# Kernel optimization log

Hardware: AMD Instinct MI355X
Metric: run time of the kernel (lower is better)

The kernel has to match this reference:

```python
import jax, jax.numpy as jnp
import numpy as np

B, S, D = 8, 1024, 768
H, DH = 8, 96          # number_of_heads, head_outdim = D // H
DFF = 4 * D            # mlp hidden
EPS = 1e-5


def _p(key, shape, scale=0.02):
    return (jax.random.normal(key, shape, dtype=jnp.float32) * scale)


def setup_inputs() -> dict:
    key = jax.random.key(0)
    ks = jax.random.split(key, 16)
    return {
        "h": jax.random.normal(ks[0], (B, S, D), dtype=jnp.float32),
        "x": jax.random.normal(ks[1], (B, S, D), dtype=jnp.float32),
        # SLN 1: scalar gamma/beta + LayerNorm affine
        "g1": jnp.ones((), jnp.float32), "be1": jnp.zeros((), jnp.float32),
        "ln1_w": jnp.ones((D,), jnp.float32), "ln1_b": jnp.zeros((D,), jnp.float32),
        # SLN 2
        "g2": jnp.ones((), jnp.float32), "be2": jnp.zeros((), jnp.float32),
        "ln2_w": jnp.ones((D,), jnp.float32), "ln2_b": jnp.zeros((D,), jnp.float32),
        # MSA projections (stored as [in, out] for x @ W)
        "Wq": _p(ks[2], (D, H * DH)), "bq": jnp.zeros((H * DH,), jnp.float32),
        "Wk": _p(ks[3], (D, H * DH)), "bk": jnp.zeros((H * DH,), jnp.float32),
        "Wv": _p(ks[4], (D, H * DH)), "bv": jnp.zeros((H * DH,), jnp.float32),
        "Wo": _p(ks[5], (H * DH, D)), "bo": jnp.zeros((D,), jnp.float32),
        # MLP: D -> 4D -> D, relu
        "W1": _p(ks[6], (D, DFF)), "b1": jnp.zeros((DFF,), jnp.float32),
        "W2": _p(ks[7], (DFF, D)), "b2": jnp.zeros((D,), jnp.float32),
    }


def _sln(h, x, gamma, beta, w, b):
    # SLN(h, x) = gamma * x * LayerNorm(h) + beta * x
    mu = jnp.mean(h, axis=-1, keepdims=True)
    var = jnp.var(h, axis=-1, keepdims=True)
    ln = (h - mu) * jax.lax.rsqrt(var + EPS) * w + b
    return gamma * x * ln + beta * x


def _l2_msa(h, Wq, bq, Wk, bk, Wv, bv, Wo, bo):
    # L2-distance multi-head self-attention (lp=2)
    def heads(W, bias):
        y = h @ W + bias                      # [B,S,H*DH]
        return y.reshape(B, S, H, DH).transpose(0, 2, 1, 3)  # [B,H,S,DH]
    q, k, v = heads(Wq, bq), heads(Wk, bk), heads(Wv, bv)
    # pairwise L2 distances via the quadratic expansion (avoids [B,H,S,S,DH])
    q2 = jnp.sum(q * q, axis=-1)              # [B,H,S]
    k2 = jnp.sum(k * k, axis=-1)              # [B,H,S]
    qk = jnp.einsum("bhsd,bhtd->bhst", q, k)  # [B,H,S,S]
    d2 = jnp.maximum(q2[..., :, None] + k2[..., None, :] - 2.0 * qk, 0.0)
    dist = jnp.sqrt(d2)                       # cdist(q, k, p=2)
    attn = jax.nn.softmax(-dist / np.sqrt(DH), axis=-1)
    out = jnp.einsum("bhst,bhtd->bhsd", attn, v)  # [B,H,S,DH]
    out = out.transpose(0, 2, 1, 3).reshape(B, S, H * DH)
    return out @ Wo + bo


def reference(h, x, g1, be1, ln1_w, ln1_b, g2, be2, ln2_w, ln2_b,
              Wq, bq, Wk, bk, Wv, bv, Wo, bo, W1, b1, W2, b2):
    h1 = _sln(h, x, g1, be1, ln1_w, ln1_b)
    htmp = _l2_msa(h1, Wq, bq, Wk, bk, Wv, bv, Wo, bo) + h   # dropout_rate=0 -> identity
    h2 = _sln(htmp, x, g2, be2, ln2_w, ln2_b)
    hf = jax.nn.relu(h2 @ W1 + b1) @ W2 + b2 + htmp
    return (x, hf)
```

## Files before the change

kernel.cpp:

```cpp
#include <hip/hip_runtime.h>
#include <math.h>

#define B_ 8
#define S_ 1024
#define D_ 768
#define H_ 8
#define DH_ 96
#define DFF_ 3072
#define NTOK (B_*S_)
#define QKVW 2304
#define EPS_ 1e-5f

typedef __attribute__((ext_vector_type(4))) float f4;
typedef __attribute__((ext_vector_type(4))) int i4;
typedef __attribute__((ext_vector_type(8))) __bf16 bf16x8;
typedef __attribute__((ext_vector_type(4))) unsigned short us4;
typedef __attribute__((ext_vector_type(8))) unsigned short us8;

static __device__ __forceinline__ unsigned short f2bf(float f) {
    unsigned int u = __builtin_bit_cast(unsigned int, f);
    u += 0x7fffu + ((u >> 16) & 1u);
    return (unsigned short)(u >> 16);
}
static __device__ __forceinline__ float bf2f(unsigned short u) {
    unsigned int x = ((unsigned int)u) << 16;
    return __builtin_bit_cast(float, x);
}

#define GLOBAL_LOAD_LDS16(g, l) \
    __builtin_amdgcn_global_load_lds((const __attribute__((address_space(1))) unsigned int*)(g), \
                                     (__attribute__((address_space(3))) unsigned int*)(l), 16, 0, 0)

__global__ __launch_bounds__(192) void sln_kernel(
    const float* __restrict__ h, const float* __restrict__ x,
    const float* __restrict__ gamma, const float* __restrict__ beta,
    const float* __restrict__ w, const float* __restrict__ bvec,
    unsigned short* __restrict__ out_bf, float* __restrict__ xcopy)
{
    int row = blockIdx.x;
    int t = threadIdx.x;
    const float4* h4 = (const float4*)(h + (size_t)row * D_);
    const float4* x4 = (const float4*)(x + (size_t)row * D_);
    float4 hv = h4[t];
    float s  = hv.x + hv.y + hv.z + hv.w;
    float ss = hv.x*hv.x + hv.y*hv.y + hv.z*hv.z + hv.w*hv.w;
    #pragma unroll
    for (int off = 32; off > 0; off >>= 1) {
        s  += __shfl_down(s, off);
        ss += __shfl_down(ss, off);
    }
    __shared__ float red[2][3];
    int wid = t >> 6;
    if ((t & 63) == 0) { red[0][wid] = s; red[1][wid] = ss; }
    __syncthreads();
    float sum   = red[0][0] + red[0][1] + red[0][2];
    float sumsq = red[1][0] + red[1][1] + red[1][2];
    float mu  = sum * (1.0f / D_);
    float var = sumsq * (1.0f / D_) - mu * mu;
    float rstd = rsqrtf(var + EPS_);
    float g = gamma[0], be = beta[0];
    float4 wv = ((const float4*)w)[t];
    float4 bv = ((const float4*)bvec)[t];
    float4 xv = x4[t];
    us4 o;
    o.x = f2bf(xv.x * (g * ((hv.x - mu) * rstd * wv.x + bv.x) + be));
    o.y = f2bf(xv.y * (g * ((hv.y - mu) * rstd * wv.y + bv.y) + be));
    o.z = f2bf(xv.z * (g * ((hv.z - mu) * rstd * wv.z + bv.z) + be));
    o.w = f2bf(xv.w * (g * ((hv.w - mu) * rstd * wv.w + bv.w) + be));
    *(us4*)(out_bf + (size_t)row * D_ + t * 4) = o;
    if (xcopy) ((float4*)(xcopy + (size_t)row * D_))[t] = xv;
}

__global__ __launch_bounds__(256) void prep_all_kernel(
    const float* __restrict__ Wq, const float* __restrict__ Wk,
    const float* __restrict__ Wv, const float* __restrict__ Wo,
    const float* __restrict__ W1, const float* __restrict__ W2,
    const float* __restrict__ bq, const float* __restrict__ bk, const float* __restrict__ bv,
    unsigned short* __restrict__ Wqkvt, unsigned short* __restrict__ Wot,
    unsigned short* __restrict__ W1t, unsigned short* __restrict__ W2t,
    float* __restrict__ bqkv)
{
    int id = blockIdx.x;
    int tx = threadIdx.x, ty = threadIdx.y;
    if (id >= 6912) {
        int i = (id - 6912) * 256 + ty * 32 + tx;
        if (i < QKVW) {
            float v = (i < 768) ? bq[i] : (i < 1536) ? bk[i - 768] : bv[i - 1536];
            bqkv[i] = v;
        }
        return;
    }
    const float* in; unsigned short* out; int K, N, nbx, rel;
    if (id < 1728)      { int m = id / 576; rel = id % 576;
                          in = (m == 0) ? Wq : (m == 1) ? Wk : Wv;
                          out = Wqkvt + (size_t)m * 768 * 768; K = 768; N = 768; nbx = 24; }
    else if (id < 2304) { rel = id - 1728; in = Wo; out = Wot;  K = 768;  N = 768;  nbx = 24; }
    else if (id < 4608) { rel = id - 2304; in = W1; out = W1t;  K = 768;  N = 3072; nbx = 96; }
    else                { rel = id - 4608; in = W2; out = W2t;  K = 3072; N = 768;  nbx = 24; }
    int n0 = (rel % nbx) * 32, k0 = (rel / nbx) * 32;
    __shared__ float tile[32][33];
    #pragma unroll
    for (int r = 0; r < 4; r++)
        tile[ty + r * 8][tx] = in[(size_t)(k0 + ty + r * 8) * N + n0 + tx];
    __syncthreads();
    #pragma unroll
    for (int r = 0; r < 4; r++)
        out[(size_t)(n0 + ty + r * 8) * K + k0 + tx] = f2bf(tile[tx][ty + r * 8]);
}

template<int OUT_BF16, int RELU>
__global__ __launch_bounds__(256) void gemm_mfma_kernel(
    const unsigned short* __restrict__ A, const unsigned short* __restrict__ Bt,
    const float* __restrict__ bias, const float* __restrict__ resid,
    void* __restrict__ Cout, int M, int N, int K)
{
    __shared__ unsigned short Asm[128 * 32];
    __shared__ unsigned short Bsm[128 * 32];

    int t = threadIdx.x;
    int lane = t & 63, wv = t >> 6;
    int wm = wv & 1, wn = wv >> 1;
    int l16 = lane & 15, quad = lane >> 4;

    int bm = blockIdx.x * 128;
    int bn = blockIdx.y * 128;

    const unsigned short* Abase = A  + (size_t)bm * K;
    const unsigned short* Bbase = Bt + (size_t)bn * K;

    int fl0 = t, fl1 = 256 + t;
    int r0s = fl0 >> 2, kc0 = (fl0 & 3) << 3;
    int r1s = fl1 >> 2, kc1 = (fl1 & 3) << 3;

    f4 acc[4][4] = {};

    for (int k0 = 0; k0 < K; k0 += 32) {
        __syncthreads();
        GLOBAL_LOAD_LDS16(Abase + (size_t)r0s * K + k0 + kc0, &Asm[fl0 * 8]);
        GLOBAL_LOAD_LDS16(Abase + (size_t)r1s * K + k0 + kc1, &Asm[fl1 * 8]);
        GLOBAL_LOAD_LDS16(Bbase + (size_t)r0s * K + k0 + kc0, &Bsm[fl0 * 8]);
        GLOBAL_LOAD_LDS16(Bbase + (size_t)r1s * K + k0 + kc1, &Bsm[fl1 * 8]);
        __syncthreads();

        bf16x8 xf[4], wf[4];
        #pragma unroll
        for (int i = 0; i < 4; i++) {
            int m = wm * 64 + i * 16 + l16;
            xf[i] = __builtin_bit_cast(bf16x8, *(const i4*)&Asm[m * 32 + quad * 8]);
        }
        #pragma unroll
        for (int j = 0; j < 4; j++) {
            int n = wn * 64 + j * 16 + l16;
            wf[j] = __builtin_bit_cast(bf16x8, *(const i4*)&Bsm[n * 32 + quad * 8]);
        }
        #pragma unroll
        for (int j = 0; j < 4; j++)
            #pragma unroll
            for (int i = 0; i < 4; i++)
                acc[j][i] = __builtin_amdgcn_mfma_f32_16x16x32_bf16(wf[j], xf[i], acc[j][i], 0, 0, 0);
    }

    #pragma unroll
    for (int i = 0; i < 4; i++) {
        int rowg = bm + wm * 64 + i * 16 + l16;
        #pragma unroll
        for (int j = 0; j < 4; j++) {
            int colg0 = bn + wn * 64 + j * 16 + quad * 4;
            f4 v = acc[j][i];
            f4 b4 = *(const f4*)&bias[colg0];
            v += b4;
            if (RELU) {
                #pragma unroll
                for (int r = 0; r < 4; r++) v[r] = fmaxf(v[r], 0.f);
            }
            if (resid) {
                f4 r4 = *(const f4*)&resid[(size_t)rowg * N + colg0];
                v += r4;
            }
            if (OUT_BF16) {
                us4 o;
                o.x = f2bf(v[0]); o.y = f2bf(v[1]); o.z = f2bf(v[2]); o.w = f2bf(v[3]);
                *(us4*)((unsigned short*)Cout + (size_t)rowg * N + colg0) = o;
            } else {
                *(f4*)((float*)Cout + (size_t)rowg * N + colg0) = v;
            }
        }
    }
}

template<int OUT_BF16, int RELU>
__global__ __launch_bounds__(256) void gemm_mfma_n64_kernel(
    const unsigned short* __restrict__ A, const unsigned short* __restrict__ Bt,
    const float* __restrict__ bias, const float* __restrict__ resid,
    void* __restrict__ Cout, int M, int N, int K)
{
    __shared__ unsigned short Asm[128 * 32];
    __shared__ unsigned short Bsm[64 * 32];

    int t = threadIdx.x;
    int lane = t & 63, wv = t >> 6;
    int wm = wv & 1, wn = wv >> 1;
    int l16 = lane & 15, quad = lane >> 4;

    int bm = blockIdx.x * 128;
    int bn = blockIdx.y * 64;

    const unsigned short* Abase = A  + (size_t)bm * K;
    const unsigned short* Bbase = Bt + (size_t)bn * K;

    int fl0 = t, fl1 = 256 + t;
    int r0s = fl0 >> 2, kc0 = (fl0 & 3) << 3;
    int r1s = fl1 >> 2, kc1 = (fl1 & 3) << 3;

    f4 acc[2][4] = {};

    for (int k0 = 0; k0 < K; k0 += 32) {
        __syncthreads();
        GLOBAL_LOAD_LDS16(Abase + (size_t)r0s * K + k0 + kc0, &Asm[fl0 * 8]);
        GLOBAL_LOAD_LDS16(Abase + (size_t)r1s * K + k0 + kc1, &Asm[fl1 * 8]);
        GLOBAL_LOAD_LDS16(Bbase + (size_t)r0s * K + k0 + kc0, &Bsm[fl0 * 8]);
        __syncthreads();

        bf16x8 xf[4], wf[2];
        #pragma unroll
        for (int i = 0; i < 4; i++) {
            int m = wm * 64 + i * 16 + l16;
            xf[i] = __builtin_bit_cast(bf16x8, *(const i4*)&Asm[m * 32 + quad * 8]);
        }
        #pragma unroll
        for (int j = 0; j < 2; j++) {
            int n = wn * 32 + j * 16 + l16;
            wf[j] = __builtin_bit_cast(bf16x8, *(const i4*)&Bsm[n * 32 + quad * 8]);
        }
        #pragma unroll
        for (int j = 0; j < 2; j++)
            #pragma unroll
            for (int i = 0; i < 4; i++)
                acc[j][i] = __builtin_amdgcn_mfma_f32_16x16x32_bf16(wf[j], xf[i], acc[j][i], 0, 0, 0);
    }

    #pragma unroll
    for (int i = 0; i < 4; i++) {
        int rowg = bm + wm * 64 + i * 16 + l16;
        #pragma unroll
        for (int j = 0; j < 2; j++) {
            int colg0 = bn + wn * 32 + j * 16 + quad * 4;
            f4 v = acc[j][i];
            f4 b4 = *(const f4*)&bias[colg0];
            v += b4;
            if (RELU) {
                #pragma unroll
                for (int r = 0; r < 4; r++) v[r] = fmaxf(v[r], 0.f);
            }
            if (resid) {
                f4 r4 = *(const f4*)&resid[(size_t)rowg * N + colg0];
                v += r4;
            }
            if (OUT_BF16) {
                us4 o;
                o.x = f2bf(v[0]); o.y = f2bf(v[1]); o.z = f2bf(v[2]); o.w = f2bf(v[3]);
                *(us4*)((unsigned short*)Cout + (size_t)rowg * N + colg0) = o;
            } else {
                *(f4*)((float*)Cout + (size_t)rowg * N + colg0) = v;
            }
        }
    }
}

__global__ __launch_bounds__(256) void norms_kernel(
    const unsigned short* __restrict__ qkv, float* __restrict__ q2g, float* __restrict__ k2g)
{
    int row = blockIdx.x;
    int t = threadIdx.x;
    int hh = t >> 5, l32 = t & 31;
    const unsigned short* base = qkv + (size_t)row * QKVW + hh * DH_ + l32 * 3;
    float qs = 0.f, ks = 0.f;
    #pragma unroll
    for (int e = 0; e < 3; e++) {
        float qv = bf2f(base[e]);
        float kv = bf2f(base[768 + e]);
        qs += qv * qv; ks += kv * kv;
    }
    #pragma unroll
    for (int off = 16; off > 0; off >>= 1) {
        qs += __shfl_xor(qs, off, 32);
        ks += __shfl_xor(ks, off, 32);
    }
    if (l32 == 0) {
        int b = row >> 10, s = row & 1023;
        int idx = (b * H_ + hh) * S_ + s;
        q2g[idx] = qs; k2g[idx] = ks;
    }
}

__global__ __launch_bounds__(256) void vtrans_kernel(
    const unsigned short* __restrict__ qkv, unsigned short* __restrict__ vt)
{
    __shared__ unsigned short Vl[64][100];
    int blk = blockIdx.x;
    int bh = blk >> 4, kt = blk & 15;
    int b = bh >> 3, hh = bh & 7;
    int t = threadIdx.x;
    int key = t >> 2, qc = t & 3;
    const unsigned short* src = qkv + ((size_t)(b * S_ + kt * 64 + key)) * QKVW + 1536 + hh * DH_;
    #pragma unroll
    for (int i = 0; i < 3; i++) {
        int chunk = qc + i * 4;
        us8 v = *(const us8*)(src + chunk * 8);
        #pragma unroll
        for (int e = 0; e < 8; e++) Vl[key][chunk * 8 + e] = v[e];
    }
    __syncthreads();
    unsigned short* dst = vt + (size_t)blk * 7168;
    #pragma unroll
    for (int r = 0; r < 3; r++) {
        int c = r * 256 + t;
        int vd = c >> 3, kc = c & 7;
        us8 o;
        #pragma unroll
        for (int j = 0; j < 8; j++) o[j] = Vl[kc * 8 + j][vd];
        *(us8*)(dst + vd * 72 + kc * 8) = o;
    }
}

__global__ __launch_bounds__(256, 4) void attn_mfma_kernel(
    const unsigned short* __restrict__ qkv,
    const unsigned short* __restrict__ vt,
    const float* __restrict__ q2g, const float* __restrict__ k2g,
    unsigned short* __restrict__ outb)
{
    __shared__ unsigned short Klds[64 * 96];
    __shared__ unsigned short Vlds[7168];
    __shared__ unsigned short Plds[4][16 * 72];

    int t = threadIdx.x;
    int lane = t & 63, w = t >> 6;
    int l16 = lane & 15, quad = lane >> 4;

    int bh = blockIdx.x >> 4;
    int qt = blockIdx.x & 15;
    int b = bh >> 3, hh = bh & 7;

    int qrow0 = qt * 64 + w * 16;

    const unsigned short* qb = qkv + ((size_t)(b * S_ + qrow0)) * QKVW + hh * DH_;
    bf16x8 qf[3];
    #pragma unroll
    for (int d = 0; d < 3; d++)
        qf[d] = __builtin_bit_cast(bf16x8,
            *(const i4*)(qb + (size_t)l16 * QKVW + d * 32 + quad * 8));

    float q2n = q2g[bh * S_ + qrow0 + l16];

    float lsum = 0.f;
    f4 Oacc[6] = {};

    const float cexp = 0.14724445f;

    const unsigned short* kgb = qkv + ((size_t)(b * S_)) * QKVW + 768 + hh * DH_;
    const unsigned short* vgb0 = vt + (size_t)(bh * 16) * 7168;

    for (int it = 0; it < 16; it++) {
        __syncthreads();
        #pragma unroll
        for (int r = 0; r < 3; r++) {
            int c = r * 256 + t;
            int key = c / 12, dc = c % 12;
            GLOBAL_LOAD_LDS16(kgb + ((size_t)(it * 64 + key)) * QKVW + dc * 8, &Klds[c * 8]);
        }
        const unsigned short* vgb = vgb0 + (size_t)it * 7168;
        #pragma unroll
        for (int r = 0; r < 3; r++)
            GLOBAL_LOAD_LDS16(vgb + (r * 256 + t) * 8, &Vlds[(r * 256 + t) * 8]);
        if (t < 128)
            GLOBAL_LOAD_LDS16(vgb + (768 + t) * 8, &Vlds[(768 + t) * 8]);
        __syncthreads();

        #pragma unroll
        for (int kt2 = 0; kt2 < 4; kt2++) {
            bf16x8 kf0 = __builtin_bit_cast(bf16x8, *(const i4*)&Klds[(kt2 * 16 + l16) * 96 + quad * 8]);
            bf16x8 kf1 = __builtin_bit_cast(bf16x8, *(const i4*)&Klds[(kt2 * 16 + l16) * 96 + 32 + quad * 8]);
            bf16x8 kf2 = __builtin_bit_cast(bf16x8, *(const i4*)&Klds[(kt2 * 16 + l16) * 96 + 64 + quad * 8]);
            f4 a = {};
            a = __builtin_amdgcn_mfma_f32_16x16x32_bf16(kf0, qf[0], a, 0, 0, 0);
            a = __builtin_amdgcn_mfma_f32_16x16x32_bf16(kf1, qf[1], a, 0, 0, 0);
            a = __builtin_amdgcn_mfma_f32_16x16x32_bf16(kf2, qf[2], a, 0, 0, 0);
            float4 k2f = *(const float4*)(k2g + bh * S_ + it * 64 + kt2 * 16 + quad * 4);
            float pk2[4] = {k2f.x + q2n, k2f.y + q2n, k2f.z + q2n, k2f.w + q2n};
            #pragma unroll
            for (int r2 = 0; r2 < 4; r2++) {
                float d2 = fmaxf(pk2[r2] - 2.f * a[r2], 0.f);
                float p = exp2f(-__builtin_amdgcn_sqrtf(d2) * cexp);
                lsum += p;
                a[r2] = p;
            }
            uint2 pkd;
            pkd.x = (unsigned)f2bf(a[0]) | ((unsigned)f2bf(a[1]) << 16);
            pkd.y = (unsigned)f2bf(a[2]) | ((unsigned)f2bf(a[3]) << 16);
            *(uint2*)&Plds[w][l16 * 72 + kt2 * 16 + quad * 4] = pkd;
        }
        bf16x8 pa0 = __builtin_bit_cast(bf16x8, *(const i4*)&Plds[w][l16 * 72 + quad * 8]);
        bf16x8 pa1 = __builtin_bit_cast(bf16x8, *(const i4*)&Plds[w][l16 * 72 + 32 + quad * 8]);
        #pragma unroll
        for (int vtl = 0; vtl < 6; vtl++) {
            bf16x8 vf0 = __builtin_bit_cast(bf16x8, *(const i4*)&Vlds[(vtl * 16 + l16) * 72 + quad * 8]);
            bf16x8 vf1 = __builtin_bit_cast(bf16x8, *(const i4*)&Vlds[(vtl * 16 + l16) * 72 + 32 + quad * 8]);
            Oacc[vtl] = __builtin_amdgcn_mfma_f32_16x16x32_bf16(pa0, vf0, Oacc[vtl], 0, 0, 0);
            Oacc[vtl] = __builtin_amdgcn_mfma_f32_16x16x32_bf16(pa1, vf1, Oacc[vtl], 0, 0, 0);
        }
    }
    lsum += __shfl_xor(lsum, 16, 64);
    lsum += __shfl_xor(lsum, 32, 64);
    float inv_l = 1.f / lsum;
    f4 iv;
    #pragma unroll
    for (int r2 = 0; r2 < 4; r2++)
        iv[r2] = __shfl(inv_l, quad * 4 + r2, 64);
    #pragma unroll
    for (int vtl = 0; vtl < 6; vtl++)
        #pragma unroll
        for (int r2 = 0; r2 < 4; r2++) {
            int row = b * S_ + qrow0 + quad * 4 + r2;
            outb[(size_t)row * D_ + hh * DH_ + vtl * 16 + l16] = f2bf(Oacc[vtl][r2] * iv[r2]);
        }
}

extern "C" void kernel_launch(void* const* d_in, const int* in_sizes, int n_in,
                              void* d_out, int out_size, void* d_ws, size_t ws_size,
                              hipStream_t stream)
{
    const float* h    = (const float*)d_in[0];
    const float* x    = (const float*)d_in[1];
    const float* g1   = (const float*)d_in[2];
    const float* be1  = (const float*)d_in[3];
    const float* ln1w = (const float*)d_in[4];
    const float* ln1b = (const float*)d_in[5];
    const float* g2   = (const float*)d_in[6];
    const float* be2  = (const float*)d_in[7];
    const float* ln2w = (const float*)d_in[8];
    const float* ln2b = (const float*)d_in[9];
    const float* Wq   = (const float*)d_in[10];
    const float* bq   = (const float*)d_in[11];
    const float* Wk   = (const float*)d_in[12];
    const float* bk   = (const float*)d_in[13];
    const float* Wv   = (const float*)d_in[14];
    const float* bv   = (const float*)d_in[15];
    const float* Wo   = (const float*)d_in[16];
    const float* bo   = (const float*)d_in[17];
    const float* W1   = (const float*)d_in[18];
    const float* b1   = (const float*)d_in[19];
    const float* W2   = (const float*)d_in[20];
    const float* b2   = (const float*)d_in[21];

    float* out = (float*)d_out;
    char* wsb = (char*)d_ws;
    const size_t ND = (size_t)NTOK * D_;

    size_t off = 0;
    unsigned short* W1t = (unsigned short*)(wsb + off); off += 4718592;
    unsigned short* W2t = (unsigned short*)(wsb + off); off += 4718592;
    float* bqkv = (float*)(wsb + off);                  off += 16384;
    float* htmp = (float*)(wsb + off);                  off += ND * 4;
    float* q2g  = (float*)(wsb + off);                  off += (size_t)B_ * H_ * S_ * 4;
    float* k2g  = (float*)(wsb + off);                  off += (size_t)B_ * H_ * S_ * 4;
    unsigned short* h2b = (unsigned short*)(wsb + off); off += ND * 2;
    size_t pool0 = off;
    unsigned short* Wqkvt = (unsigned short*)(wsb + off); off += 3538944;
    unsigned short* Wot   = (unsigned short*)(wsb + off); off += 1179648;
    unsigned short* h1b   = (unsigned short*)(wsb + off); off += ND * 2;
    unsigned short* vtg   = (unsigned short*)(wsb + off); off += (size_t)1024 * 14336;
    unsigned short* qkvb  = (unsigned short*)(wsb + off); off += (size_t)NTOK * QKVW * 2;
    unsigned short* attnb   = h1b;
    unsigned short* hiddenb = (unsigned short*)(wsb + pool0);

    prep_all_kernel<<<6921, dim3(32, 8), 0, stream>>>(
        Wq, Wk, Wv, Wo, W1, W2, bq, bk, bv, Wqkvt, Wot, W1t, W2t, bqkv);

    sln_kernel<<<NTOK, 192, 0, stream>>>(h, x, g1, be1, ln1w, ln1b, h1b, out);

    gemm_mfma_kernel<1, 0><<<dim3(NTOK/128, QKVW/128), 256, 0, stream>>>(
        h1b, Wqkvt, bqkv, nullptr, qkvb, NTOK, QKVW, D_);

    norms_kernel<<<NTOK, 256, 0, stream>>>(qkvb, q2g, k2g);
    vtrans_kernel<<<1024, 256, 0, stream>>>(qkvb, vtg);

    attn_mfma_kernel<<<1024, 256, 0, stream>>>(qkvb, vtg, q2g, k2g, attnb);

    gemm_mfma_n64_kernel<0, 0><<<dim3(NTOK/128, D_/64), 256, 0, stream>>>(
        attnb, Wot, bo, h, htmp, NTOK, D_, D_);

    sln_kernel<<<NTOK, 192, 0, stream>>>(htmp, x, g2, be2, ln2w, ln2b, h2b, nullptr);

    gemm_mfma_kernel<1, 1><<<dim3(NTOK/128, DFF_/128), 256, 0, stream>>>(
        h2b, W1t, b1, nullptr, hiddenb, NTOK, DFF_, D_);
    gemm_mfma_n64_kernel<0, 0><<<dim3(NTOK/128, D_/64), 256, 0, stream>>>(
        hiddenb, W2t, b2, htmp, out + ND, NTOK, D_, DFF_);

    (void)in_sizes; (void)n_in; (void)out_size; (void)ws_size;
}
```

Before: 452.1 us.

## Double-buffer GEMM LDS tiles with XOR swizzle and deeper K step for n64 kernel

```diff
diff --git a/kernel.cpp b/kernel.cpp
--- a/kernel.cpp
+++ b/kernel.cpp
@@ -114,8 +114,8 @@
     const float* __restrict__ bias, const float* __restrict__ resid,
     void* __restrict__ Cout, int M, int N, int K)
 {
-    __shared__ unsigned short Asm[128 * 32];
-    __shared__ unsigned short Bsm[128 * 32];
+    __shared__ unsigned short Asm[2][128 * 32];
+    __shared__ unsigned short Bsm[2][128 * 32];
 
     int t = threadIdx.x;
     int lane = t & 63, wv = t >> 6;
@@ -129,35 +129,49 @@
     const unsigned short* Bbase = Bt + (size_t)bn * K;
 
     int fl0 = t, fl1 = 256 + t;
-    int r0s = fl0 >> 2, kc0 = (fl0 & 3) << 3;
-    int r1s = fl1 >> 2, kc1 = (fl1 & 3) << 3;
+    int r0 = fl0 >> 2, lg0 = (fl0 ^ (fl0 >> 3)) & 3;
+    int r1 = fl1 >> 2, lg1 = (fl1 ^ (fl1 >> 3)) & 3;
 
     f4 acc[4][4] = {};
 
-    for (int k0 = 0; k0 < K; k0 += 32) {
-        __syncthreads();
-        GLOBAL_LOAD_LDS16(Abase + (size_t)r0s * K + k0 + kc0, &Asm[fl0 * 8]);
-        GLOBAL_LOAD_LDS16(Abase + (size_t)r1s * K + k0 + kc1, &Asm[fl1 * 8]);
-        GLOBAL_LOAD_LDS16(Bbase + (size_t)r0s * K + k0 + kc0, &Bsm[fl0 * 8]);
-        GLOBAL_LOAD_LDS16(Bbase + (size_t)r1s * K + k0 + kc1, &Bsm[fl1 * 8]);
-        __syncthreads();
+    GLOBAL_LOAD_LDS16(Abase + (size_t)r0 * K + lg0 * 8, &Asm[0][fl0 * 8]);
+    GLOBAL_LOAD_LDS16(Abase + (size_t)r1 * K + lg1 * 8, &Asm[0][fl1 * 8]);
+    GLOBAL_LOAD_LDS16(Bbase + (size_t)r0 * K + lg0 * 8, &Bsm[0][fl0 * 8]);
+    GLOBAL_LOAD_LDS16(Bbase + (size_t)r1 * K + lg1 * 8, &Bsm[0][fl1 * 8]);
+    __syncthreads();
+
+    int nk = K >> 5;
+    int cur = 0;
+    for (int it = 0; it < nk; ++it) {
+        if (it + 1 < nk) {
+            int k0 = (it + 1) << 5;
+            GLOBAL_LOAD_LDS16(Abase + (size_t)r0 * K + k0 + lg0 * 8, &Asm[cur ^ 1][fl0 * 8]);
+            GLOBAL_LOAD_LDS16(Abase + (size_t)r1 * K + k0 + lg1 * 8, &Asm[cur ^ 1][fl1 * 8]);
+            GLOBAL_LOAD_LDS16(Bbase + (size_t)r0 * K + k0 + lg0 * 8, &Bsm[cur ^ 1][fl0 * 8]);
+            GLOBAL_LOAD_LDS16(Bbase + (size_t)r1 * K + k0 + lg1 * 8, &Bsm[cur ^ 1][fl1 * 8]);
+        }
 
         bf16x8 xf[4], wf[4];
         #pragma unroll
         for (int i = 0; i < 4; i++) {
             int m = wm * 64 + i * 16 + l16;
-            xf[i] = __builtin_bit_cast(bf16x8, *(const i4*)&Asm[m * 32 + quad * 8]);
+            int p = (quad ^ (m >> 1)) & 3;
+            xf[i] = __builtin_bit_cast(bf16x8, *(const i4*)&Asm[cur][m * 32 + p * 8]);
         }
         #pragma unroll
         for (int j = 0; j < 4; j++) {
             int n = wn * 64 + j * 16 + l16;
-            wf[j] = __builtin_bit_cast(bf16x8, *(const i4*)&Bsm[n * 32 + quad * 8]);
+            int p = (quad ^ (n >> 1)) & 3;
+            wf[j] = __builtin_bit_cast(bf16x8, *(const i4*)&Bsm[cur][n * 32 + p * 8]);
         }
         #pragma unroll
         for (int j = 0; j < 4; j++)
             #pragma unroll
             for (int i = 0; i < 4; i++)
                 acc[j][i] = __builtin_amdgcn_mfma_f32_16x16x32_bf16(wf[j], xf[i], acc[j][i], 0, 0, 0);
+
+        __syncthreads();
+        cur ^= 1;
     }
 
     #pragma unroll
@@ -194,8 +208,8 @@
     const float* __restrict__ bias, const float* __restrict__ resid,
     void* __restrict__ Cout, int M, int N, int K)
 {
-    __shared__ unsigned short Asm[128 * 32];
-    __shared__ unsigned short Bsm[64 * 32];
+    __shared__ unsigned short Asm[2][128 * 64];
+    __shared__ unsigned short Bsm[2][64 * 64];
 
     int t = threadIdx.x;
     int lane = t & 63, wv = t >> 6;
@@ -208,35 +222,65 @@
     const unsigned short* Abase = A  + (size_t)bm * K;
     const unsigned short* Bbase = Bt + (size_t)bn * K;
 
-    int fl0 = t, fl1 = 256 + t;
-    int r0s = fl0 >> 2, kc0 = (fl0 & 3) << 3;
-    int r1s = fl1 >> 2, kc1 = (fl1 & 3) << 3;
+    int ar[4], alg[4], br[2], blg[2];
+    #pragma unroll
+    for (int i = 0; i < 4; i++) {
+        int fl = t + i * 256;
+        ar[i] = fl >> 3; alg[i] = (fl ^ (fl >> 3)) & 7;
+    }
+    #pragma unroll
+    for (int i = 0; i < 2; i++) {
+        int fl = t + i * 256;
+        br[i] = fl >> 3; blg[i] = (fl ^ (fl >> 3)) & 7;
+    }
 
     f4 acc[2][4] = {};
 
-    for (int k0 = 0; k0 < K; k0 += 32) {
+    #pragma unroll
+    for (int i = 0; i < 4; i++)
+        GLOBAL_LOAD_LDS16(Abase + (size_t)ar[i] * K + alg[i] * 8, &Asm[0][(t + i * 256) * 8]);
+    #pragma unroll
+    for (int i = 0; i < 2; i++)
+        GLOBAL_LOAD_LDS16(Bbase + (size_t)br[i] * K + blg[i] * 8, &Bsm[0][(t + i * 256) * 8]);
+    __syncthreads();
+
+    int nk = K >> 6;
+    int cur = 0;
+    for (int it = 0; it < nk; ++it) {
+        if (it + 1 < nk) {
+            int k0 = (it + 1) << 6;
+            #pragma unroll
+            for (int i = 0; i < 4; i++)
+                GLOBAL_LOAD_LDS16(Abase + (size_t)ar[i] * K + k0 + alg[i] * 8, &Asm[cur ^ 1][(t + i * 256) * 8]);
+            #pragma unroll
+            for (int i = 0; i < 2; i++)
+                GLOBAL_LOAD_LDS16(Bbase + (size_t)br[i] * K + k0 + blg[i] * 8, &Bsm[cur ^ 1][(t + i * 256) * 8]);
+        }
+
+        #pragma unroll
+        for (int kk = 0; kk < 2; kk++) {
+            bf16x8 xf[4], wf[2];
+            #pragma unroll
+            for (int i = 0; i < 4; i++) {
+                int m = wm * 64 + i * 16 + l16;
+                int p = ((kk * 4 + quad) ^ (m & 7)) & 7;
+                xf[i] = __builtin_bit_cast(bf16x8, *(const i4*)&Asm[cur][m * 64 + p * 8]);
+            }
+            #pragma unroll
+            for (int j = 0; j < 2; j++) {
+                int n = wn * 32 + j * 16 + l16;
+                int p = ((kk * 4 + quad) ^ (n & 7)) & 7;
+                wf[j] = __builtin_bit_cast(bf16x8, *(const i4*)&Bsm[cur][n * 64 + p * 8]);
+            }
+            #pragma unroll
+            for (int j = 0; j < 2; j++)
+                #pragma unroll
+                for (int i = 0; i < 4; i++)
+                    acc[j][i] = __builtin_amdgcn_mfma_f32_16x16x32_bf16(wf[j], xf[i], acc[j][i], 0, 0, 0);
+        }
+
         __syncthreads();
-        GLOBAL_LOAD_LDS16(Abase + (size_t)r0s * K + k0 + kc0, &Asm[fl0 * 8]);
-        GLOBAL_LOAD_LDS16(Abase + (size_t)r1s * K + k0 + kc1, &Asm[fl1 * 8]);
-        GLOBAL_LOAD_LDS16(Bbase + (size_t)r0s * K + k0 + kc0, &Bsm[fl0 * 8]);
-        __syncthreads();
-
-        bf16x8 xf[4], wf[2];
-        #pragma unroll
-        for (int i = 0; i < 4; i++) {
-            int m = wm * 64 + i * 16 + l16;
-            xf[i] = __builtin_bit_cast(bf16x8, *(const i4*)&Asm[m * 32 + quad * 8]);
-        }
-        #pragma unroll
-        for (int j = 0; j < 2; j++) {
-            int n = wn * 32 + j * 16 + l16;
-            wf[j] = __builtin_bit_cast(bf16x8, *(const i4*)&Bsm[n * 32 + quad * 8]);
-        }
-        #pragma unroll
-        for (int j = 0; j < 2; j++)
-            #pragma unroll
-            for (int i = 0; i < 4; i++)
-                acc[j][i] = __builtin_amdgcn_mfma_f32_16x16x32_bf16(wf[j], xf[i], acc[j][i], 0, 0, 0);
+        cur ^= 1;
     }
 
     #pragma unroll
```

Measured after the change: 424.2 us. 6.2% less time.
